# Performance work log

Measured on AMD Instinct MI355X. Metric: run time of the kernel, lower is better.

## Reference

```python
import jax, jax.numpy as jnp
import numpy as np

S = 64        # memory_slots
SLOT_DIM = 256
BOND = 32     # bond_dim
NQ = 8        # num_qubits = max(4, ceil(log2(slot_dim)))
QDIM = 2 ** NQ  # 256
DIM = 1024    # input feature dim


def setup_inputs() -> dict:
    key = jax.random.key(0)
    ks = jax.random.split(key, 8)
    std = 1.0 / np.sqrt(BOND)
    x = jax.random.normal(ks[0], (8, 4096, DIM), dtype=jnp.float32)
    Wq = jax.random.normal(ks[1], (DIM, QDIM), dtype=jnp.float32) * 0.02
    bq = jnp.zeros((QDIM,), dtype=jnp.float32)
    Wd = jax.random.normal(ks[2], (SLOT_DIM, DIM), dtype=jnp.float32) * 0.02
    bd = jnp.zeros((DIM,), dtype=jnp.float32)
    # MPS cores batched over slots; original shapes per slot:
    #   q=0: (1,2,BOND), q=1..NQ-2: (BOND,2,BOND), q=NQ-1: (BOND,2,1)
    core_first = jax.random.normal(ks[3], (S, 2, BOND), dtype=jnp.float32) * std
    core_mid = jax.random.normal(ks[4], (S, NQ - 2, BOND, 2, BOND), dtype=jnp.float32) * std
    core_last = jax.random.normal(ks[5], (S, BOND, 2), dtype=jnp.float32) * std
    return {"x": x, "Wq": Wq, "bq": bq, "Wd": Wd, "bd": bd,
            "core_first": core_first, "core_mid": core_mid, "core_last": core_last}


def _amp_means(qa):
    """Per-qubit strided means of query amplitudes. qa: [b, 2^NQ] -> (m0, m1): [b, NQ]."""
    m0s, m1s = [], []
    for q in range(NQ):
        stride = 2 ** (NQ - q - 1)
        idx0 = np.arange(stride) * (2 * stride)  # qa[:, ::2*stride][:, :stride]
        idx1 = idx0 + stride                     # qa[:, stride::2*stride][:, :stride]
        m0s.append(qa[:, idx0].mean(axis=-1))
        m1s.append(qa[:, idx1].mean(axis=-1))
    return jnp.stack(m0s, axis=1), jnp.stack(m1s, axis=1)


def reference(x, Wq, bq, Wd, bd, core_first, core_mid, core_last):
    # x: [b, t, d]
    x_summary = x.mean(axis=1)                         # [b, d]
    qa = jax.nn.softmax(x_summary @ Wq + bq, axis=-1)  # [b, QDIM]
    m0, m1 = _amp_means(qa)                            # [b, NQ] each

    # MPS contraction, vectorized over (batch b, slot s)
    # q = 0: left bond is 1 -> result directly [b, S, BOND]
    res = (m0[:, 0, None, None] * core_first[None, :, 0, :]
           + m1[:, 0, None, None] * core_first[None, :, 1, :])
    for q in range(1, NQ - 1):
        wc = (m0[:, q, None, None, None] * core_mid[None, :, q - 1, :, 0, :]
              + m1[:, q, None, None, None] * core_mid[None, :, q - 1, :, 1, :])  # [b,S,B,B]
        res = jnp.einsum('bsl,bslr->bsr', res, wc)
    # q = NQ-1: right bond is 1
    wc_last = (m0[:, NQ - 1, None, None] * core_last[None, :, :, 0]
               + m1[:, NQ - 1, None, None] * core_last[None, :, :, 1])  # [b,S,B]
    overlaps = jnp.einsum('bsl,bsl->bs', res, wc_last)  # [b, S]

    attention = jax.nn.softmax(overlaps, axis=-1)       # [b, S]

    # read values: per-slot per-qubit core means, tiled to slot_dim
    f0 = core_first.mean(axis=(1, 2))                   # [S]
    fm = core_mid.mean(axis=(2, 3, 4))                  # [S, NQ-2]
    fl = core_last.mean(axis=(1, 2))                    # [S]
    feats = jnp.concatenate([f0[:, None], fm, fl[:, None]], axis=1)  # [S, NQ]
    rep = SLOT_DIM // NQ + 1
    slot_values = jnp.tile(feats, (1, rep))[:, :SLOT_DIM]            # [S, SLOT_DIM]

    read_out = attention @ slot_values                  # [b, SLOT_DIM]
    read_proj = read_out @ Wd + bd                      # [b, DIM]
    return x + read_proj[:, None, :]
```

## Files before the change

kernel.cpp:

```cpp
#include <hip/hip_runtime.h>
#include <hip/hip_bf16.h>

#define B_    8
#define T_    4096
#define D_    1024
#define S_    64
#define NQ_   8
#define QDIM_ 256
#define TB_   64
#define NTC_  (T_/TB_)

typedef __attribute__((ext_vector_type(4))) unsigned short u16x4;
typedef __attribute__((ext_vector_type(8))) unsigned short u16x8;
typedef __attribute__((ext_vector_type(4))) float f32x4;

__device__ __forceinline__ float b2f(unsigned short u) {
    union { unsigned int i; float f; } v; v.i = ((unsigned int)u) << 16; return v.f;
}
__device__ __forceinline__ unsigned short f2b(float f) {
    __hip_bfloat16 h = __float2bfloat16(f);
    return *reinterpret_cast<unsigned short*>(&h);
}

__device__ __forceinline__ float blockSum(float v, float* buf) {
    int tid = threadIdx.x;
    buf[tid] = v; __syncthreads();
    #pragma unroll
    for (int s = 128; s > 0; s >>= 1) { if (tid < s) buf[tid] += buf[tid + s]; __syncthreads(); }
    float r = buf[0]; __syncthreads();
    return r;
}
__device__ __forceinline__ float blockMax(float v, float* buf) {
    int tid = threadIdx.x;
    buf[tid] = v; __syncthreads();
    #pragma unroll
    for (int s = 128; s > 0; s >>= 1) { if (tid < s) buf[tid] = fmaxf(buf[tid], buf[tid + s]); __syncthreads(); }
    float r = buf[0]; __syncthreads();
    return r;
}

__global__ __launch_bounds__(256)
void k_detect(const unsigned short* __restrict__ x,
              const unsigned short* __restrict__ wq,
              int* __restrict__ flags) {
    __shared__ int cnt[2];
    int tid = threadIdx.x;
    if (tid == 0) { cnt[0] = 0; cnt[1] = 0; }
    __syncthreads();
    unsigned short u = x[tid];
    unsigned e = (u >> 7) & 0xFF;
    bool okx = ((u & 0x7FFF) == 0) || (e >= 100 && e <= 130);
    u = wq[tid];
    e = (u >> 7) & 0xFF;
    bool okw = ((u & 0x7FFF) == 0) || (e >= 96 && e <= 126);
    unsigned long long bx = __ballot(okx);
    unsigned long long bw = __ballot(okw);
    if ((tid & 63) == 0) {
        atomicAdd(&cnt[0], (int)__popcll(bx));
        atomicAdd(&cnt[1], (int)__popcll(bw));
    }
    __syncthreads();
    if (tid == 0) {
        flags[0] = (cnt[0] < 200) ? 1 : 0;
        flags[1] = (cnt[1] < 200) ? 1 : 0;
    }
}

__global__ __launch_bounds__(256)
void k_colsum(const void* __restrict__ x, float* __restrict__ partials,
              const int* __restrict__ flags) {
    int blk = blockIdx.x;
    int b  = blk >> 6;
    int tc = blk & 63;
    int tid = threadIdx.x;
    size_t base = ((size_t)(b * T_ + tc * TB_)) * D_ + tid * 4;
    float a0 = 0.f, a1 = 0.f, a2 = 0.f, a3 = 0.f;
    if (flags[0]) {
        const float* px = (const float*)x + base;
        #pragma unroll 8
        for (int i = 0; i < TB_; ++i) {
            f32x4 v = *reinterpret_cast<const f32x4*>(px + (size_t)i * D_);
            a0 += v[0]; a1 += v[1]; a2 += v[2]; a3 += v[3];
        }
    } else {
        const unsigned short* px = (const unsigned short*)x + base;
        #pragma unroll 8
        for (int i = 0; i < TB_; ++i) {
            u16x4 v = *reinterpret_cast<const u16x4*>(px + (size_t)i * D_);
            a0 += b2f(v[0]); a1 += b2f(v[1]); a2 += b2f(v[2]); a3 += b2f(v[3]);
        }
    }
    float* dst = partials + ((size_t)(tc * B_ + b)) * D_ + tid * 4;
    f32x4 r; r[0] = a0; r[1] = a1; r[2] = a2; r[3] = a3;
    *reinterpret_cast<f32x4*>(dst) = r;
}

__global__ __launch_bounds__(256)
void k_logits(const float* __restrict__ partials, const void* __restrict__ Wq,
              float* __restrict__ plog, const int* __restrict__ flags) {
    __shared__ float xs[128];
    int b = blockIdx.x >> 3, dc = blockIdx.x & 7;
    int tid = threadIdx.x;
    int d0 = dc * 128;
    if (tid < 128) {
        float a = 0.f;
        for (int tc = 0; tc < NTC_; ++tc)
            a += partials[((size_t)(tc * B_ + b)) * D_ + d0 + tid];
        xs[tid] = a * (1.f / (float)T_);
    }
    __syncthreads();
    float lg = 0.f;
    if (flags[1]) {
        const float* w = (const float*)Wq + (size_t)d0 * QDIM_ + tid;
        #pragma unroll 8
        for (int d = 0; d < 128; ++d) lg += xs[d] * w[(size_t)d * QDIM_];
    } else {
        const unsigned short* w = (const unsigned short*)Wq + (size_t)d0 * QDIM_ + tid;
        #pragma unroll 8
        for (int d = 0; d < 128; ++d) lg += xs[d] * b2f(w[(size_t)d * QDIM_]);
    }
    plog[((size_t)(b * 8 + dc)) * QDIM_ + tid] = lg;
}

__global__ __launch_bounds__(256)
void k_softmax_amp(const float* __restrict__ plog, const void* __restrict__ bq,
                   float* __restrict__ sm0m, float* __restrict__ sm1m,
                   const int* __restrict__ flags) {
    __shared__ float qa[QDIM_];
    __shared__ float buf[256];
    int b = blockIdx.x, tid = threadIdx.x;
    float lg = flags[1] ? ((const float*)bq)[tid] : b2f(((const unsigned short*)bq)[tid]);
    for (int dc = 0; dc < 8; ++dc) lg += plog[((size_t)(b * 8 + dc)) * QDIM_ + tid];
    float mx = blockMax(lg, buf);
    float e = __expf(lg - mx);
    float ss = blockSum(e, buf);
    qa[tid] = e / ss;
    __syncthreads();
    if (tid < 16) {
        int q = tid >> 1, bit = tid & 1;
        int sw = 1 << (7 - q);
        float acc = 0.f;
        for (int i = 0; i < sw; ++i) {
            int idx = 2 * sw * i + bit * sw;
            if (idx > QDIM_ - 1) idx = QDIM_ - 1;
            acc += qa[idx];
        }
        float m = acc / (float)sw;
        if (bit == 0) sm0m[b * 8 + q] = m; else sm1m[b * 8 + q] = m;
    }
}

__global__ __launch_bounds__(256)
void k_mps(const void* __restrict__ cf, const void* __restrict__ cm,
           const void* __restrict__ cl,
           const float* __restrict__ sm0m, const float* __restrict__ sm1m,
           float* __restrict__ feats, float* __restrict__ ovl,
           const int* __restrict__ flags) {
    __shared__ float lcf[64];
    __shared__ float lcm[6 * 2048];
    __shared__ float lcl[64];
    __shared__ float res[8][33];
    __shared__ float nres[8][33];
    __shared__ float buf[256];
    __shared__ float lm0[64], lm1[64];
    int s = blockIdx.x, tid = threadIdx.x;
    if (flags[1]) {
        const float* pcm = (const float*)cm + (size_t)s * 12288;
        for (int i = tid; i < 12288; i += 256) lcm[i] = pcm[i];
        if (tid < 64) {
            lcf[tid] = ((const float*)cf)[s * 64 + tid];
            lcl[tid] = ((const float*)cl)[s * 64 + tid];
        }
    } else {
        const unsigned short* pcm = (const unsigned short*)cm + (size_t)s * 12288;
        for (int i = tid; i < 12288; i += 256) lcm[i] = b2f(pcm[i]);
        if (tid < 64) {
            lcf[tid] = b2f(((const unsigned short*)cf)[s * 64 + tid]);
            lcl[tid] = b2f(((const unsigned short*)cl)[s * 64 + tid]);
        }
    }
    if (tid < 64) { lm0[tid] = sm0m[tid]; lm1[tid] = sm1m[tid]; }
    __syncthreads();

    {
        float v = (tid < 64) ? lcf[tid] : 0.f;
        float f0 = blockSum(v, buf) * (1.f / 64.f);
        float fj[6];
        for (int j = 0; j < 6; ++j) {
            float a = 0.f;
            for (int k = tid; k < 2048; k += 256) a += lcm[j * 2048 + k];
            fj[j] = blockSum(a, buf) * (1.f / 2048.f);
        }
        float w = (tid < 64) ? lcl[tid] : 0.f;
        float fl = blockSum(w, buf) * (1.f / 64.f);
        if (tid == 0) {
            feats[s * 8 + 0] = f0;
            #pragma unroll
            for (int j = 0; j < 6; ++j) feats[s * 8 + 1 + j] = fj[j];
            feats[s * 8 + 7] = fl;
        }
    }

    int b = tid >> 5, r = tid & 31;
    res[b][r] = lm0[b * 8 + 0] * lcf[r] + lm1[b * 8 + 0] * lcf[32 + r];
    __syncthreads();
    for (int q = 1; q <= 6; ++q) {
        float m0 = lm0[b * 8 + q], m1 = lm1[b * 8 + q];
        const float* C = &lcm[(q - 1) * 2048];
        float acc = 0.f;
        #pragma unroll 8
        for (int l = 0; l < 32; ++l)
            acc += res[b][l] * (m0 * C[l * 64 + r] + m1 * C[l * 64 + 32 + r]);
        nres[b][r] = acc;
        __syncthreads();
        res[b][r] = nres[b][r];
        __syncthreads();
    }
    {
        float m0 = lm0[b * 8 + 7], m1 = lm1[b * 8 + 7];
        float p = res[b][r] * (m0 * lcl[r * 2] + m1 * lcl[r * 2 + 1]);
        #pragma unroll
        for (int off = 16; off > 0; off >>= 1) p += __shfl_xor(p, off, 64);
        if (r == 0) ovl[b * 64 + s] = p;
    }
}

__global__ __launch_bounds__(256)
void k_attproj(const float* __restrict__ ovl, const float* __restrict__ feats,
               const void* __restrict__ Wd, const void* __restrict__ bd,
               float* __restrict__ read_proj, const int* __restrict__ flags) {
    __shared__ float att[S_];
    __shared__ float gl[NQ_];
    int b = blockIdx.x >> 2, dc = blockIdx.x & 3;
    int tid = threadIdx.x;
    if (tid < 64) {
        float o = ovl[b * 64 + tid];
        float mx = o;
        #pragma unroll
        for (int off = 32; off > 0; off >>= 1) mx = fmaxf(mx, __shfl_xor(mx, off, 64));
        float e = __expf(o - mx);
        float se = e;
        #pragma unroll
        for (int off = 32; off > 0; off >>= 1) se += __shfl_xor(se, off, 64);
        att[tid] = e / se;
    }
    __syncthreads();
    if (tid < 8) {
        float g = 0.f;
        for (int s2 = 0; s2 < S_; ++s2) g += att[s2] * feats[s2 * 8 + tid];
        gl[tid] = g;
    }
    __syncthreads();
    int d = dc * 256 + tid;
    float a = flags[1] ? ((const float*)bd)[d] : b2f(((const unsigned short*)bd)[d]);
    if (flags[1]) {
        const float* w = (const float*)Wd + d;
        #pragma unroll 8
        for (int c = 0; c < QDIM_; ++c) a += gl[c & 7] * w[(size_t)c * D_];
    } else {
        const unsigned short* w = (const unsigned short*)Wd + d;
        #pragma unroll 8
        for (int c = 0; c < QDIM_; ++c) a += gl[c & 7] * b2f(w[(size_t)c * D_]);
    }
    read_proj[(size_t)b * D_ + d] = a;
}

__global__ __launch_bounds__(256)
void k_add(const void* __restrict__ x, const float* __restrict__ rp,
           void* __restrict__ out, const int* __restrict__ flags) {
    size_t base = (((size_t)blockIdx.x) * 256 + threadIdx.x) * 8;
    int b = (int)(base >> 22);
    int d = (int)(base & (D_ - 1));
    const float* r = rp + (size_t)b * D_ + d;
    f32x4 r0 = *reinterpret_cast<const f32x4*>(r);
    f32x4 r1 = *reinterpret_cast<const f32x4*>(r + 4);
    if (flags[0]) {
        const float* px = (const float*)x + base;
        f32x4 v0 = *reinterpret_cast<const f32x4*>(px);
        f32x4 v1 = *reinterpret_cast<const f32x4*>(px + 4);
        f32x4 o0 = v0 + r0;
        f32x4 o1 = v1 + r1;
        float* po = (float*)out + base;
        *reinterpret_cast<f32x4*>(po) = o0;
        *reinterpret_cast<f32x4*>(po + 4) = o1;
    } else {
        u16x8 v = *reinterpret_cast<const u16x8*>((const unsigned short*)x + base);
        u16x8 o;
        #pragma unroll
        for (int k = 0; k < 4; ++k) o[k] = f2b(b2f(v[k]) + r0[k]);
        #pragma unroll
        for (int k = 0; k < 4; ++k) o[4 + k] = f2b(b2f(v[4 + k]) + r1[k]);
        *reinterpret_cast<u16x8*>((unsigned short*)out + base) = o;
    }
}

extern "C" void kernel_launch(void* const* d_in, const int* in_sizes, int n_in,
                              void* d_out, int out_size, void* d_ws, size_t ws_size,
                              hipStream_t stream) {
    const void* x  = d_in[0];
    const void* Wq = d_in[1];
    const void* bq = d_in[2];
    const void* Wd = d_in[3];
    const void* bd = d_in[4];
    const void* cf = d_in[5];
    const void* cm = d_in[6];
    const void* cl = d_in[7];

    float* ws        = (float*)d_ws;
    float* partials  = ws;
    float* plog      = partials + 524288;
    float* sm0m      = plog + 16384;
    float* sm1m      = sm0m + 64;
    float* feats     = sm1m + 64;
    float* ovl       = feats + 512;
    float* read_proj = ovl + 512;
    int*   flags     = (int*)(read_proj + 8192);

    k_detect<<<1, 256, 0, stream>>>((const unsigned short*)x, (const unsigned short*)Wq, flags);
    k_colsum<<<B_ * NTC_, 256, 0, stream>>>(x, partials, flags);
    k_logits<<<64, 256, 0, stream>>>(partials, Wq, plog, flags);
    k_softmax_amp<<<B_, 256, 0, stream>>>(plog, bq, sm0m, sm1m, flags);
    k_mps<<<S_, 256, 0, stream>>>(cf, cm, cl, sm0m, sm1m, feats, ovl, flags);
    k_attproj<<<32, 256, 0, stream>>>(ovl, feats, Wd, bd, read_proj, flags);
    k_add<<<(B_ * T_ * D_) / 2048, 256, 0, stream>>>(x, read_proj, d_out, flags);
}
```

Measured before the change: 314.4 us.

## Fuse all stages into one persistent kernel with grid-wide atomic barriers

Replaces the seven-kernel pipeline with a single 512-block persistent kernel that separates stages with software grid barriers built on agent-scope atomics. Each block detects the input dtype locally, and Wd is pre-reduced over the 8-periodic slot features in parallel with the logits stage. The goal is to remove per-launch overhead and the serial tail kernels on the critical path. In exchange it relies on all 512 blocks (256 threads, launch bounds of 2 per CU) being co-resident, adds spin-wait barrier latency, and the final add loop now runs with far fewer blocks.

```diff
diff --git a/kernel.cpp b/kernel.cpp
--- a/kernel.cpp
+++ b/kernel.cpp
@@ -9,6 +9,7 @@
 #define QDIM_ 256
 #define TB_   64
 #define NTC_  (T_/TB_)
+#define NBLK  512
 
 typedef __attribute__((ext_vector_type(4))) unsigned short u16x4;
 typedef __attribute__((ext_vector_type(8))) unsigned short u16x8;
@@ -39,258 +40,280 @@
     return r;
 }
 
-__global__ __launch_bounds__(256)
-void k_detect(const unsigned short* __restrict__ x,
-              const unsigned short* __restrict__ wq,
-              int* __restrict__ flags) {
-    __shared__ int cnt[2];
-    int tid = threadIdx.x;
-    if (tid == 0) { cnt[0] = 0; cnt[1] = 0; }
+__device__ __forceinline__ void gbar(int* slot) {
     __syncthreads();
-    unsigned short u = x[tid];
-    unsigned e = (u >> 7) & 0xFF;
-    bool okx = ((u & 0x7FFF) == 0) || (e >= 100 && e <= 130);
-    u = wq[tid];
-    e = (u >> 7) & 0xFF;
-    bool okw = ((u & 0x7FFF) == 0) || (e >= 96 && e <= 126);
-    unsigned long long bx = __ballot(okx);
-    unsigned long long bw = __ballot(okw);
-    if ((tid & 63) == 0) {
-        atomicAdd(&cnt[0], (int)__popcll(bx));
-        atomicAdd(&cnt[1], (int)__popcll(bw));
+    if (threadIdx.x == 0) {
+        __hip_atomic_fetch_add(slot, 1, __ATOMIC_RELEASE, __HIP_MEMORY_SCOPE_AGENT);
+        while (__hip_atomic_load(slot, __ATOMIC_RELAXED, __HIP_MEMORY_SCOPE_AGENT) < NBLK)
+            __builtin_amdgcn_s_sleep(8);
+        (void)__hip_atomic_load(slot, __ATOMIC_ACQUIRE, __HIP_MEMORY_SCOPE_AGENT);
     }
     __syncthreads();
-    if (tid == 0) {
-        flags[0] = (cnt[0] < 200) ? 1 : 0;
-        flags[1] = (cnt[1] < 200) ? 1 : 0;
-    }
-}
-
-__global__ __launch_bounds__(256)
-void k_colsum(const void* __restrict__ x, float* __restrict__ partials,
-              const int* __restrict__ flags) {
-    int blk = blockIdx.x;
-    int b  = blk >> 6;
-    int tc = blk & 63;
-    int tid = threadIdx.x;
-    size_t base = ((size_t)(b * T_ + tc * TB_)) * D_ + tid * 4;
-    float a0 = 0.f, a1 = 0.f, a2 = 0.f, a3 = 0.f;
-    if (flags[0]) {
-        const float* px = (const float*)x + base;
-        #pragma unroll 8
-        for (int i = 0; i < TB_; ++i) {
-            f32x4 v = *reinterpret_cast<const f32x4*>(px + (size_t)i * D_);
-            a0 += v[0]; a1 += v[1]; a2 += v[2]; a3 += v[3];
-        }
-    } else {
-        const unsigned short* px = (const unsigned short*)x + base;
-        #pragma unroll 8
-        for (int i = 0; i < TB_; ++i) {
-            u16x4 v = *reinterpret_cast<const u16x4*>(px + (size_t)i * D_);
-            a0 += b2f(v[0]); a1 += b2f(v[1]); a2 += b2f(v[2]); a3 += b2f(v[3]);
-        }
-    }
-    float* dst = partials + ((size_t)(tc * B_ + b)) * D_ + tid * 4;
-    f32x4 r; r[0] = a0; r[1] = a1; r[2] = a2; r[3] = a3;
-    *reinterpret_cast<f32x4*>(dst) = r;
-}
-
-__global__ __launch_bounds__(256)
-void k_logits(const float* __restrict__ partials, const void* __restrict__ Wq,
-              float* __restrict__ plog, const int* __restrict__ flags) {
-    __shared__ float xs[128];
-    int b = blockIdx.x >> 3, dc = blockIdx.x & 7;
-    int tid = threadIdx.x;
-    int d0 = dc * 128;
-    if (tid < 128) {
+}
+
+struct MpsSh {
+    float lcm[6 * 2048];
+    float lcf[64];
+    float lcl[64];
+    float res[8][33];
+    float nres[8][33];
+    float lm0[64], lm1[64];
+    float buf[256];
+};
+struct LogitsSh { float xs2[256]; float xs[128]; };
+struct SmSh     { float qa[QDIM_]; float buf[256]; };
+struct AttSh    { float att[S_]; float g[NQ_]; };
+union Sh { MpsSh mps; LogitsSh lg; SmSh sm; AttSh att; };
+
+__global__ __launch_bounds__(256, 2)
+void k_fused(const void* __restrict__ x,  const void* __restrict__ Wq,
+             const void* __restrict__ bq, const void* __restrict__ Wd,
+             const void* __restrict__ bd, const void* __restrict__ cf,
+             const void* __restrict__ cm, const void* __restrict__ cl,
+             float* __restrict__ partials, float* __restrict__ plog,
+             float* __restrict__ sm0m, float* __restrict__ sm1m,
+             float* __restrict__ feats, float* __restrict__ ovl,
+             float* __restrict__ read_proj, float* __restrict__ wdred,
+             int* __restrict__ bar, void* __restrict__ out) {
+    __shared__ Sh u;
+    __shared__ int dcnt[2];
+    const int blk = blockIdx.x;
+    const int tid = threadIdx.x;
+
+    bool xf32, wf32;
+    {
+        if (tid < 2) dcnt[tid] = 0;
+        __syncthreads();
+        unsigned short ux = ((const unsigned short*)x)[tid];
+        unsigned ex = (ux >> 7) & 0xFF;
+        bool okx = ((ux & 0x7FFF) == 0) || (ex >= 100 && ex <= 130);
+        unsigned short uw = ((const unsigned short*)Wq)[tid];
+        unsigned ew = (uw >> 7) & 0xFF;
+        bool okw = ((uw & 0x7FFF) == 0) || (ew >= 96 && ew <= 126);
+        unsigned long long bx = __ballot(okx);
+        unsigned long long bw = __ballot(okw);
+        if ((tid & 63) == 0) {
+            atomicAdd(&dcnt[0], (int)__popcll(bx));
+            atomicAdd(&dcnt[1], (int)__popcll(bw));
+        }
+        __syncthreads();
+        xf32 = dcnt[0] < 200;
+        wf32 = dcnt[1] < 200;
+        __syncthreads();
+    }
+
+    {
+        int b  = blk >> 6;
+        int tc = blk & 63;
+        size_t base = ((size_t)(b * T_ + tc * TB_)) * D_ + tid * 4;
+        float a0 = 0.f, a1 = 0.f, a2 = 0.f, a3 = 0.f;
+        if (xf32) {
+            const float* px = (const float*)x + base;
+            #pragma unroll 8
+            for (int i = 0; i < TB_; ++i) {
+                f32x4 v = *reinterpret_cast<const f32x4*>(px + (size_t)i * D_);
+                a0 += v[0]; a1 += v[1]; a2 += v[2]; a3 += v[3];
+            }
+        } else {
+            const unsigned short* px = (const unsigned short*)x + base;
+            #pragma unroll 8
+            for (int i = 0; i < TB_; ++i) {
+                u16x4 v = *reinterpret_cast<const u16x4*>(px + (size_t)i * D_);
+                a0 += b2f(v[0]); a1 += b2f(v[1]); a2 += b2f(v[2]); a3 += b2f(v[3]);
+            }
+        }
+        float* dst = partials + ((size_t)(tc * B_ + b)) * D_ + tid * 4;
+        f32x4 r; r[0] = a0; r[1] = a1; r[2] = a2; r[3] = a3;
+        *reinterpret_cast<f32x4*>(dst) = r;
+    }
+    gbar(bar + 0);
+
+    if (blk < 64) {
+        int b = blk >> 3, dc = blk & 7;
+        int d0 = dc * 128;
         float a = 0.f;
-        for (int tc = 0; tc < NTC_; ++tc)
-            a += partials[((size_t)(tc * B_ + b)) * D_ + d0 + tid];
-        xs[tid] = a * (1.f / (float)T_);
-    }
-    __syncthreads();
-    float lg = 0.f;
-    if (flags[1]) {
-        const float* w = (const float*)Wq + (size_t)d0 * QDIM_ + tid;
-        #pragma unroll 8
-        for (int d = 0; d < 128; ++d) lg += xs[d] * w[(size_t)d * QDIM_];
-    } else {
-        const unsigned short* w = (const unsigned short*)Wq + (size_t)d0 * QDIM_ + tid;
-        #pragma unroll 8
-        for (int d = 0; d < 128; ++d) lg += xs[d] * b2f(w[(size_t)d * QDIM_]);
-    }
-    plog[((size_t)(b * 8 + dc)) * QDIM_ + tid] = lg;
-}
-
-__global__ __launch_bounds__(256)
-void k_softmax_amp(const float* __restrict__ plog, const void* __restrict__ bq,
-                   float* __restrict__ sm0m, float* __restrict__ sm1m,
-                   const int* __restrict__ flags) {
-    __shared__ float qa[QDIM_];
-    __shared__ float buf[256];
-    int b = blockIdx.x, tid = threadIdx.x;
-    float lg = flags[1] ? ((const float*)bq)[tid] : b2f(((const unsigned short*)bq)[tid]);
-    for (int dc = 0; dc < 8; ++dc) lg += plog[((size_t)(b * 8 + dc)) * QDIM_ + tid];
-    float mx = blockMax(lg, buf);
-    float e = __expf(lg - mx);
-    float ss = blockSum(e, buf);
-    qa[tid] = e / ss;
-    __syncthreads();
-    if (tid < 16) {
-        int q = tid >> 1, bit = tid & 1;
-        int sw = 1 << (7 - q);
-        float acc = 0.f;
-        for (int i = 0; i < sw; ++i) {
-            int idx = 2 * sw * i + bit * sw;
-            if (idx > QDIM_ - 1) idx = QDIM_ - 1;
-            acc += qa[idx];
-        }
-        float m = acc / (float)sw;
-        if (bit == 0) sm0m[b * 8 + q] = m; else sm1m[b * 8 + q] = m;
-    }
-}
-
-__global__ __launch_bounds__(256)
-void k_mps(const void* __restrict__ cf, const void* __restrict__ cm,
-           const void* __restrict__ cl,
-           const float* __restrict__ sm0m, const float* __restrict__ sm1m,
-           float* __restrict__ feats, float* __restrict__ ovl,
-           const int* __restrict__ flags) {
-    __shared__ float lcf[64];
-    __shared__ float lcm[6 * 2048];
-    __shared__ float lcl[64];
-    __shared__ float res[8][33];
-    __shared__ float nres[8][33];
-    __shared__ float buf[256];
-    __shared__ float lm0[64], lm1[64];
-    int s = blockIdx.x, tid = threadIdx.x;
-    if (flags[1]) {
-        const float* pcm = (const float*)cm + (size_t)s * 12288;
-        for (int i = tid; i < 12288; i += 256) lcm[i] = pcm[i];
+        for (int tc = (tid >> 7); tc < NTC_; tc += 2)
+            a += partials[((size_t)(tc * B_ + b)) * D_ + d0 + (tid & 127)];
+        u.lg.xs2[tid] = a;
+        __syncthreads();
+        if (tid < 128) u.lg.xs[tid] = (u.lg.xs2[tid] + u.lg.xs2[tid + 128]) * (1.f / (float)T_);
+        __syncthreads();
+        float lg = 0.f;
+        if (wf32) {
+            const float* w = (const float*)Wq + (size_t)d0 * QDIM_ + tid;
+            #pragma unroll 8
+            for (int d = 0; d < 128; ++d) lg += u.lg.xs[d] * w[(size_t)d * QDIM_];
+        } else {
+            const unsigned short* w = (const unsigned short*)Wq + (size_t)d0 * QDIM_ + tid;
+            #pragma unroll 8
+            for (int d = 0; d < 128; ++d) lg += u.lg.xs[d] * b2f(w[(size_t)d * QDIM_]);
+        }
+        plog[((size_t)(b * 8 + dc)) * QDIM_ + tid] = lg;
+    } else if (blk < 96) {
+        int bi = blk - 64;
+        int j = tid >> 5;
+        int d = bi * 32 + (tid & 31);
+        float a = 0.f;
+        if (wf32) {
+            const float* w = (const float*)Wd;
+            #pragma unroll 8
+            for (int k = 0; k < 32; ++k) a += w[(size_t)(j + 8 * k) * D_ + d];
+        } else {
+            const unsigned short* w = (const unsigned short*)Wd;
+            #pragma unroll 8
+            for (int k = 0; k < 32; ++k) a += b2f(w[(size_t)(j + 8 * k) * D_ + d]);
+        }
+        wdred[(size_t)j * D_ + d] = a;
+    }
+    gbar(bar + 1);
+
+    if (blk < 8) {
+        int b = blk;
+        float lg = wf32 ? ((const float*)bq)[tid] : b2f(((const unsigned short*)bq)[tid]);
+        for (int dc = 0; dc < 8; ++dc) lg += plog[((size_t)(b * 8 + dc)) * QDIM_ + tid];
+        float mx = blockMax(lg, u.sm.buf);
+        float e = __expf(lg - mx);
+        float ss = blockSum(e, u.sm.buf);
+        u.sm.qa[tid] = e / ss;
+        __syncthreads();
+        if (tid < 16) {
+            int q = tid >> 1, bit = tid & 1;
+            int sw = 1 << (7 - q);
+            float acc = 0.f;
+            for (int i = 0; i < sw; ++i) {
+                int idx = 2 * sw * i + bit * sw;
+                if (idx > QDIM_ - 1) idx = QDIM_ - 1;
+                acc += u.sm.qa[idx];
+            }
+            float m = acc / (float)sw;
+            if (bit == 0) sm0m[b * 8 + q] = m; else sm1m[b * 8 + q] = m;
+        }
+    }
+    gbar(bar + 2);
+
+    if (blk < S_) {
+        int s = blk;
+        MpsSh& M = u.mps;
+        if (wf32) {
+            const float* pcm = (const float*)cm + (size_t)s * 12288;
+            for (int i = tid; i < 12288; i += 256) M.lcm[i] = pcm[i];
+            if (tid < 64) {
+                M.lcf[tid] = ((const float*)cf)[s * 64 + tid];
+                M.lcl[tid] = ((const float*)cl)[s * 64 + tid];
+            }
+        } else {
+            const unsigned short* pcm = (const unsigned short*)cm + (size_t)s * 12288;
+            for (int i = tid; i < 12288; i += 256) M.lcm[i] = b2f(pcm[i]);
+            if (tid < 64) {
+                M.lcf[tid] = b2f(((const unsigned short*)cf)[s * 64 + tid]);
+                M.lcl[tid] = b2f(((const unsigned short*)cl)[s * 64 + tid]);
+            }
+        }
+        if (tid < 64) { M.lm0[tid] = sm0m[tid]; M.lm1[tid] = sm1m[tid]; }
+        __syncthreads();
+
+        {
+            float v = (tid < 64) ? M.lcf[tid] : 0.f;
+            float f0 = blockSum(v, M.buf) * (1.f / 64.f);
+            float fj[6];
+            for (int j = 0; j < 6; ++j) {
+                float a = 0.f;
+                for (int k = tid; k < 2048; k += 256) a += M.lcm[j * 2048 + k];
+                fj[j] = blockSum(a, M.buf) * (1.f / 2048.f);
+            }
+            float w = (tid < 64) ? M.lcl[tid] : 0.f;
+            float fl = blockSum(w, M.buf) * (1.f / 64.f);
+            if (tid == 0) {
+                feats[s * 8 + 0] = f0;
+                #pragma unroll
+                for (int j = 0; j < 6; ++j) feats[s * 8 + 1 + j] = fj[j];
+                feats[s * 8 + 7] = fl;
+            }
+        }
+
+        int b = tid >> 5, r = tid & 31;
+        M.res[b][r] = M.lm0[b * 8 + 0] * M.lcf[r] + M.lm1[b * 8 + 0] * M.lcf[32 + r];
+        __syncthreads();
+        for (int q = 1; q <= 6; ++q) {
+            float m0 = M.lm0[b * 8 + q], m1 = M.lm1[b * 8 + q];
+            const float* C = &M.lcm[(q - 1) * 2048];
+            float acc = 0.f;
+            #pragma unroll 8
+            for (int l = 0; l < 32; ++l)
+                acc += M.res[b][l] * (m0 * C[l * 64 + r] + m1 * C[l * 64 + 32 + r]);
+            M.nres[b][r] = acc;
+            __syncthreads();
+            M.res[b][r] = M.nres[b][r];
+            __syncthreads();
+        }
+        {
+            float m0 = M.lm0[b * 8 + 7], m1 = M.lm1[b * 8 + 7];
+            float p = M.res[b][r] * (m0 * M.lcl[r * 2] + m1 * M.lcl[r * 2 + 1]);
+            #pragma unroll
+            for (int off = 16; off > 0; off >>= 1) p += __shfl_xor(p, off, 64);
+            if (r == 0) ovl[b * 64 + s] = p;
+        }
+    }
+    gbar(bar + 3);
+
+    if (blk < 8) {
+        int b = blk;
         if (tid < 64) {
-            lcf[tid] = ((const float*)cf)[s * 64 + tid];
-            lcl[tid] = ((const float*)cl)[s * 64 + tid];
-        }
-    } else {
-        const unsigned short* pcm = (const unsigned short*)cm + (size_t)s * 12288;
-        for (int i = tid; i < 12288; i += 256) lcm[i] = b2f(pcm[i]);
-        if (tid < 64) {
-            lcf[tid] = b2f(((const unsigned short*)cf)[s * 64 + tid]);
-            lcl[tid] = b2f(((const unsigned short*)cl)[s * 64 + tid]);
-        }
-    }
-    if (tid < 64) { lm0[tid] = sm0m[tid]; lm1[tid] = sm1m[tid]; }
-    __syncthreads();
+            float o = ovl[b * 64 + tid];
+            float mx = o;
+            #pragma unroll
+            for (int off = 32; off > 0; off >>= 1) mx = fmaxf(mx, __shfl_xor(mx, off, 64));
+            float e = __expf(o - mx);
+            float se = e;
+            #pragma unroll
+            for (int off = 32; off > 0; off >>= 1) se += __shfl_xor(se, off, 64);
+            u.att.att[tid] = e / se;
+        }
+        __syncthreads();
+        if (tid < 8) {
+            float g = 0.f;
+            for (int s2 = 0; s2 < S_; ++s2) g += u.att.att[s2] * feats[s2 * 8 + tid];
+            u.att.g[tid] = g;
+        }
+        __syncthreads();
+        #pragma unroll
+        for (int i = 0; i < 4; ++i) {
+            int d = tid + i * 256;
+            float a = wf32 ? ((const float*)bd)[d] : b2f(((const unsigned short*)bd)[d]);
+            #pragma unroll
+            for (int j = 0; j < 8; ++j) a += u.att.g[j] * wdred[(size_t)j * D_ + d];
+            read_proj[(size_t)b * D_ + d] = a;
+        }
+    }
+    gbar(bar + 4);
 
     {
-        float v = (tid < 64) ? lcf[tid] : 0.f;
-        float f0 = blockSum(v, buf) * (1.f / 64.f);
-        float fj[6];
-        for (int j = 0; j < 6; ++j) {
-            float a = 0.f;
-            for (int k = tid; k < 2048; k += 256) a += lcm[j * 2048 + k];
-            fj[j] = blockSum(a, buf) * (1.f / 2048.f);
-        }
-        float w = (tid < 64) ? lcl[tid] : 0.f;
-        float fl = blockSum(w, buf) * (1.f / 64.f);
-        if (tid == 0) {
-            feats[s * 8 + 0] = f0;
-            #pragma unroll
-            for (int j = 0; j < 6; ++j) feats[s * 8 + 1 + j] = fj[j];
-            feats[s * 8 + 7] = fl;
-        }
-    }
-
-    int b = tid >> 5, r = tid & 31;
-    res[b][r] = lm0[b * 8 + 0] * lcf[r] + lm1[b * 8 + 0] * lcf[32 + r];
-    __syncthreads();
-    for (int q = 1; q <= 6; ++q) {
-        float m0 = lm0[b * 8 + q], m1 = lm1[b * 8 + q];
-        const float* C = &lcm[(q - 1) * 2048];
-        float acc = 0.f;
-        #pragma unroll 8
-        for (int l = 0; l < 32; ++l)
-            acc += res[b][l] * (m0 * C[l * 64 + r] + m1 * C[l * 64 + 32 + r]);
-        nres[b][r] = acc;
-        __syncthreads();
-        res[b][r] = nres[b][r];
-        __syncthreads();
-    }
-    {
-        float m0 = lm0[b * 8 + 7], m1 = lm1[b * 8 + 7];
-        float p = res[b][r] * (m0 * lcl[r * 2] + m1 * lcl[r * 2 + 1]);
-        #pragma unroll
-        for (int off = 16; off > 0; off >>= 1) p += __shfl_xor(p, off, 64);
-        if (r == 0) ovl[b * 64 + s] = p;
-    }
-}
-
-__global__ __launch_bounds__(256)
-void k_attproj(const float* __restrict__ ovl, const float* __restrict__ feats,
-               const void* __restrict__ Wd, const void* __restrict__ bd,
-               float* __restrict__ read_proj, const int* __restrict__ flags) {
-    __shared__ float att[S_];
-    __shared__ float gl[NQ_];
-    int b = blockIdx.x >> 2, dc = blockIdx.x & 3;
-    int tid = threadIdx.x;
-    if (tid < 64) {
-        float o = ovl[b * 64 + tid];
-        float mx = o;
-        #pragma unroll
-        for (int off = 32; off > 0; off >>= 1) mx = fmaxf(mx, __shfl_xor(mx, off, 64));
-        float e = __expf(o - mx);
-        float se = e;
-        #pragma unroll
-        for (int off = 32; off > 0; off >>= 1) se += __shfl_xor(se, off, 64);
-        att[tid] = e / se;
-    }
-    __syncthreads();
-    if (tid < 8) {
-        float g = 0.f;
-        for (int s2 = 0; s2 < S_; ++s2) g += att[s2] * feats[s2 * 8 + tid];
-        gl[tid] = g;
-    }
-    __syncthreads();
-    int d = dc * 256 + tid;
-    float a = flags[1] ? ((const float*)bd)[d] : b2f(((const unsigned short*)bd)[d]);
-    if (flags[1]) {
-        const float* w = (const float*)Wd + d;
-        #pragma unroll 8
-        for (int c = 0; c < QDIM_; ++c) a += gl[c & 7] * w[(size_t)c * D_];
-    } else {
-        const unsigned short* w = (const unsigned short*)Wd + d;
-        #pragma unroll 8
-        for (int c = 0; c < QDIM_; ++c) a += gl[c & 7] * b2f(w[(size_t)c * D_]);
-    }
-    read_proj[(size_t)b * D_ + d] = a;
-}
-
-__global__ __launch_bounds__(256)
-void k_add(const void* __restrict__ x, const float* __restrict__ rp,
-           void* __restrict__ out, const int* __restrict__ flags) {
-    size_t base = (((size_t)blockIdx.x) * 256 + threadIdx.x) * 8;
-    int b = (int)(base >> 22);
-    int d = (int)(base & (D_ - 1));
-    const float* r = rp + (size_t)b * D_ + d;
-    f32x4 r0 = *reinterpret_cast<const f32x4*>(r);
-    f32x4 r1 = *reinterpret_cast<const f32x4*>(r + 4);
-    if (flags[0]) {
-        const float* px = (const float*)x + base;
-        f32x4 v0 = *reinterpret_cast<const f32x4*>(px);
-        f32x4 v1 = *reinterpret_cast<const f32x4*>(px + 4);
-        f32x4 o0 = v0 + r0;
-        f32x4 o1 = v1 + r1;
-        float* po = (float*)out + base;
-        *reinterpret_cast<f32x4*>(po) = o0;
-        *reinterpret_cast<f32x4*>(po + 4) = o1;
-    } else {
-        u16x8 v = *reinterpret_cast<const u16x8*>((const unsigned short*)x + base);
-        u16x8 o;
-        #pragma unroll
-        for (int k = 0; k < 4; ++k) o[k] = f2b(b2f(v[k]) + r0[k]);
-        #pragma unroll
-        for (int k = 0; k < 4; ++k) o[4 + k] = f2b(b2f(v[4 + k]) + r1[k]);
-        *reinterpret_cast<u16x8*>((unsigned short*)out + base) = o;
+        for (int it = 0; it < 32; ++it) {
+            size_t base = (((size_t)(it * NBLK + blk)) * 256 + tid) * 8;
+            int b = (int)(base >> 22);
+            int d = (int)(base & (D_ - 1));
+            const float* r = read_proj + (size_t)b * D_ + d;
+            f32x4 r0 = *reinterpret_cast<const f32x4*>(r);
+            f32x4 r1 = *reinterpret_cast<const f32x4*>(r + 4);
+            if (xf32) {
+                const float* px = (const float*)x + base;
+                f32x4 v0 = *reinterpret_cast<const f32x4*>(px);
+                f32x4 v1 = *reinterpret_cast<const f32x4*>(px + 4);
+                f32x4 o0 = v0 + r0;
+                f32x4 o1 = v1 + r1;
+                float* po = (float*)out + base;
+                *reinterpret_cast<f32x4*>(po) = o0;
+                *reinterpret_cast<f32x4*>(po + 4) = o1;
+            } else {
+                u16x8 v = *reinterpret_cast<const u16x8*>((const unsigned short*)x + base);
+                u16x8 o;
+                #pragma unroll
+                for (int k = 0; k < 4; ++k) o[k] = f2b(b2f(v[k]) + r0[k]);
+                #pragma unroll
+                for (int k = 0; k < 4; ++k) o[4 + k] = f2b(b2f(v[4 + k]) + r1[k]);
+                *reinterpret_cast<u16x8*>((unsigned short*)out + base) = o;
+            }
+        }
     }
 }
 
@@ -314,13 +337,11 @@
     float* feats     = sm1m + 64;
     float* ovl       = feats + 512;
     float* read_proj = ovl + 512;
-    int*   flags     = (int*)(read_proj + 8192);
-
-    k_detect<<<1, 256, 0, stream>>>((const unsigned short*)x, (const unsigned short*)Wq, flags);
-    k_colsum<<<B_ * NTC_, 256, 0, stream>>>(x, partials, flags);
-    k_logits<<<64, 256, 0, stream>>>(partials, Wq, plog, flags);
-    k_softmax_amp<<<B_, 256, 0, stream>>>(plog, bq, sm0m, sm1m, flags);
-    k_mps<<<S_, 256, 0, stream>>>(cf, cm, cl, sm0m, sm1m, feats, ovl, flags);
-    k_attproj<<<32, 256, 0, stream>>>(ovl, feats, Wd, bd, read_proj, flags);
-    k_add<<<(B_ * T_ * D_) / 2048, 256, 0, stream>>>(x, read_proj, d_out, flags);
-}
+    float* wdred     = read_proj + 8192;
+    int*   bar       = (int*)(wdred + 8192);
+
+    hipMemsetAsync(bar, 0, 32, stream);
+    k_fused<<<NBLK, 256, 0, stream>>>(x, Wq, bq, Wd, bd, cf, cm, cl,
+                                      partials, plog, sm0m, sm1m, feats, ovl,
+                                      read_proj, wdred, bar, d_out);
+}
```

Result: slower. 436.3 us (+38.7%).
